# Performance work log

Measured on AMD Instinct MI355X. Metric: run time of the kernel, lower is better.

The kernel has to match this reference:

```python
import math
import jax, jax.numpy as jnp
import numpy as np

B, S, D, H = 4, 2048, 1024, 16
HD = D // H
NEG = float(jnp.finfo(jnp.float16).min)  # matches torch.finfo(torch.float16).min

def setup_inputs() -> dict:
    key = jax.random.key(0)
    ks = jax.random.split(key, 10)
    s = 1.0 / math.sqrt(D)
    return {
        "x": jax.random.normal(ks[0], (B, S, D), jnp.float32),
        "mask": jax.random.randint(ks[1], (B, 1, S, S), 0, 2).astype(bool),
        "Wq": jax.random.normal(ks[2], (D, D), jnp.float32) * s,
        "bq": jnp.zeros((D,), jnp.float32),
        "Wk": jax.random.normal(ks[3], (D, D), jnp.float32) * s,
        "bk": jnp.zeros((D,), jnp.float32),
        "Wv": jax.random.normal(ks[4], (D, D), jnp.float32) * s,
        "bv": jnp.zeros((D,), jnp.float32),
        "Wf": jax.random.normal(ks[5], (D, D), jnp.float32) * s,
        "bf": jnp.zeros((D,), jnp.float32),
    }

def reference(x, mask, Wq, bq, Wk, bk, Wv, bv, Wf, bf):
    b, s, d = x.shape
    # QKV projections (torch Linear: y = x @ W.T + b)
    q = (x @ Wq.T + bq).reshape(b, s, H, HD).transpose(0, 2, 1, 3)  # [b,h,s,hd]
    k = (x @ Wk.T + bk).reshape(b, s, H, HD).transpose(0, 2, 1, 3)
    v = (x @ Wv.T + bv).reshape(b, s, H, HD).transpose(0, 2, 1, 3)
    scores = jnp.einsum('bhqd,bhkd->bhqk', q, k) / math.sqrt(HD)
    scores = jnp.where(mask, scores, NEG)  # masked_fill_(~mask, fp16 min)
    p = jax.nn.softmax(scores, axis=-1)    # dropout is identity (eval / drop_rate=0)
    h = jnp.einsum('bhqk,bhkd->bhqd', p, v).transpose(0, 2, 1, 3).reshape(b, s, d)
    return h @ Wf.T + bf
```

## Files before the change

kernel.cpp:

```cpp
#include <hip/hip_runtime.h>
#include <math.h>

constexpr int S = 2048, D = 1024, H = 16;
constexpr float QSCL = 0.18033688011112042f;

typedef __attribute__((ext_vector_type(8))) short bf16x8;
typedef __attribute__((ext_vector_type(4))) short s16x4;
typedef __attribute__((ext_vector_type(4))) float f32x4;
typedef __attribute__((ext_vector_type(16))) float f32x16;

#define MFMA16(a,b,c) __builtin_amdgcn_mfma_f32_16x16x32_bf16(a,b,c,0,0,0)
#define MFMA32(a,b,c) __builtin_amdgcn_mfma_f32_32x32x16_bf16(a,b,c,0,0,0)

#if __has_builtin(__builtin_amdgcn_exp2f)
#define EXP2(x) __builtin_amdgcn_exp2f(x)
#else
#define EXP2(x) exp2f(x)
#endif

#define GLDS16(g, l) __builtin_amdgcn_global_load_lds( \
    (const __attribute__((address_space(1))) unsigned*)(const void*)(g), \
    (__attribute__((address_space(3))) unsigned*)(void*)(l), 16, 0, 0)

__device__ inline short f2bf(float f) {
    union { float f; unsigned u; } c; c.f = f;
    unsigned u = c.u + 0x7fffu + ((c.u >> 16) & 1u);
    return (short)(u >> 16);
}

__global__ __launch_bounds__(256)
void conv_pack(const float* __restrict__ x,  const float* __restrict__ wq,
               const float* __restrict__ wk, const float* __restrict__ wv,
               const float* __restrict__ wf,
               short* __restrict__ xb,  short* __restrict__ wqb,
               short* __restrict__ wkb, short* __restrict__ wvb,
               short* __restrict__ wfb)
{
    int i = blockIdx.x * 256 + threadIdx.x;
    const float* s; short* d; int o;
    if (i < 2097152) { s = x; d = xb; o = i; }
    else {
        int j = i - 2097152; int wsel = j >> 18; o = j & 262143;
        s = wsel == 0 ? wq : wsel == 1 ? wk : wsel == 2 ? wv : wf;
        d = wsel == 0 ? wqb : wsel == 1 ? wkb : wsel == 2 ? wvb : wfb;
    }
    float4 v = ((const float4*)s)[o];
    s16x4 r; r.x = f2bf(v.x); r.y = f2bf(v.y); r.z = f2bf(v.z); r.w = f2bf(v.w);
    ((s16x4*)d)[o] = r;
}

__global__ __launch_bounds__(256)
void conv_maskcol(const int* __restrict__ m, unsigned* __restrict__ o)
{
    int gid = blockIdx.x * 256 + threadIdx.x;
    int lane = gid & 63;
    int tile = (gid >> 6) & 31;
    int grp  = (gid >> 11) & 63;
    int bb   = gid >> 17;
    int qrow = grp * 32 + (lane & 31);
    int h = lane >> 5;
    const int* base = m + (size_t)bb * S * S + (size_t)qrow * S + tile * 64 + 4 * h;
    unsigned wbits = 0;
#pragma unroll
    for (int a = 0; a < 8; ++a) {
        int4 v = *(const int4*)(base + 8 * (a & 3) + 32 * (a >> 2));
        wbits |= (v.x != 0 ? 1u : 0u) << (4 * a);
        wbits |= (v.y != 0 ? 1u : 0u) << (4 * a + 1);
        wbits |= (v.z != 0 ? 1u : 0u) << (4 * a + 2);
        wbits |= (v.w != 0 ? 1u : 0u) << (4 * a + 3);
    }
    o[gid] = wbits;
}

__global__ __launch_bounds__(256, 3)
void qkv_mfma(const short* __restrict__ xb, const short* __restrict__ wcat,
              const float* __restrict__ bq, const float* __restrict__ bk,
              const float* __restrict__ bv,
              short* __restrict__ qo, short* __restrict__ ko, short* __restrict__ vto)
{
    __shared__ short As[128 * 64];
    __shared__ short Bs[128 * 64];
    const int t = threadIdx.x, lane = t & 63;
    const int w = __builtin_amdgcn_readfirstlane(t >> 6);
    const int lr = lane & 15, lg = lane >> 4;
    const int wr = w >> 1, wc = w & 1;
    const int m0 = blockIdx.x * 128, n0 = blockIdx.y * 128;

    const int srow = t >> 3;
    const int scol = ((t & 7) ^ (srow & 7)) * 8;
    const short* asrc = xb   + (size_t)(m0 + srow) * 1024 + scol;
    const short* bsrc = wcat + (size_t)(n0 + srow) * 1024 + scol;
    char* aldst = (char*)As + w * 1024;
    char* bldst = (char*)Bs + w * 1024;

    f32x4 z = {0.f, 0.f, 0.f, 0.f};
    f32x4 acc[4][4];
#pragma unroll
    for (int i = 0; i < 4; ++i)
#pragma unroll
        for (int jj = 0; jj < 4; ++jj) acc[i][jj] = z;

    for (int kt = 0; kt < 1024; kt += 64) {
        __syncthreads();
        GLDS16(asrc + kt,             aldst);
        GLDS16(asrc + kt + 32 * 1024, aldst + 4096);
        GLDS16(asrc + kt + 64 * 1024, aldst + 8192);
        GLDS16(asrc + kt + 96 * 1024, aldst + 12288);
        GLDS16(bsrc + kt,             bldst);
        GLDS16(bsrc + kt + 32 * 1024, bldst + 4096);
        GLDS16(bsrc + kt + 64 * 1024, bldst + 8192);
        GLDS16(bsrc + kt + 96 * 1024, bldst + 12288);
        __syncthreads();
#pragma unroll
        for (int ks = 0; ks < 2; ++ks) {
            bf16x8 af[4], bfr[4];
#pragma unroll
            for (int fi = 0; fi < 4; ++fi) {
                const int ra = wr * 64 + fi * 16 + lr;
                af[fi] = *(const bf16x8*)((const char*)As + ra * 128 +
                          ((ks * 64 + lg * 16) ^ ((ra & 7) << 4)));
                const int rb = wc * 64 + fi * 16 + lr;
                bfr[fi] = *(const bf16x8*)((const char*)Bs + rb * 128 +
                          ((ks * 64 + lg * 16) ^ ((rb & 7) << 4)));
            }
#pragma unroll
            for (int fi = 0; fi < 4; ++fi)
#pragma unroll
                for (int fj = 0; fj < 4; ++fj)
                    acc[fi][fj] = MFMA16(af[fi], bfr[fj], acc[fi][fj]);
        }
    }

    const int bb = m0 >> 11;
    const int ssb = (m0 & (S - 1)) + wr * 64 + lg * 4;
    const int mat = n0 >> 10;
    const int nbase = (n0 & 1023) + wc * 64;

    if (mat == 0) {
#pragma unroll
        for (int fj = 0; fj < 4; ++fj) {
            const int nl = nbase + fj * 16 + lr, hh = nl >> 6, hd = nl & 63;
            const float bi = bq[nl];
#pragma unroll
            for (int fi = 0; fi < 4; ++fi)
#pragma unroll
                for (int r = 0; r < 4; ++r)
                    qo[(((size_t)bb * H + hh) * S + ssb + fi * 16 + r) * 64 + hd] =
                        f2bf((acc[fi][fj][r] + bi) * QSCL);
        }
    } else if (mat == 1) {
#pragma unroll
        for (int fj = 0; fj < 4; ++fj) {
            const int nl = nbase + fj * 16 + lr, hh = nl >> 6, hd = nl & 63;
            const float bi = bk[nl];
#pragma unroll
            for (int fi = 0; fi < 4; ++fi)
#pragma unroll
                for (int r = 0; r < 4; ++r)
                    ko[(((size_t)bb * H + hh) * S + ssb + fi * 16 + r) * 64 + hd] =
                        f2bf(acc[fi][fj][r] + bi);
        }
    } else {
#pragma unroll
        for (int fj = 0; fj < 4; ++fj) {
            const int nl = nbase + fj * 16 + lr, hh = nl >> 6, hd = nl & 63;
            const float bi = bv[nl];
#pragma unroll
            for (int fi = 0; fi < 4; ++fi) {
                s16x4 pk;
#pragma unroll
                for (int r = 0; r < 4; ++r) pk[r] = f2bf(acc[fi][fj][r] + bi);
                *(s16x4*)(vto + (((size_t)bb * H + hh) * 64 + hd) * S + ssb + fi * 16) = pk;
            }
        }
    }
}

__global__ __launch_bounds__(256, 3)
void attn_mfma8(const short* __restrict__ qg, const short* __restrict__ kg,
                const short* __restrict__ vtg,
                const unsigned* __restrict__ mcol,
                short* __restrict__ hc)
{
    __shared__ short Kl[2][64 * 64];
    __shared__ short Vl[2][64 * 64];

    const int t = threadIdx.x, lane = t & 63;
    const int w = __builtin_amdgcn_readfirstlane(t >> 6);
    const int l31 = lane & 31, h = lane >> 5;

    const int id = blockIdx.x;
    const int xcd = id & 7, j = id >> 3;
    const int bh = xcd + 8 * (j >> 4);
    const int q0 = (j & 15) * 128;
    const int bb = bh >> 4, hh = bh & 15;

    const short* qb  = qg  + (size_t)bh * S * 64;
    const short* kb  = kg  + (size_t)bh * S * 64;
    const short* vtb = vtg + (size_t)bh * 64 * S;
    const unsigned* mc = mcol + ((size_t)(bb * 64 + (q0 >> 5) + w)) * 32 * 64 + lane;

    const int qrow = q0 + w * 32 + l31;
    bf16x8 qf[4];
#pragma unroll
    for (int ds = 0; ds < 4; ++ds)
        qf[ds] = *(const bf16x8*)(qb + (size_t)qrow * 64 + ds * 16 + 8 * h);

    const int sk = t >> 3;
    const int soff = (((t & 7) * 16) ^ ((sk & 7) << 4)) >> 1;
    const int rbyte = l31 * 128;
    const int sz = (lane & 7) << 4;

    f32x16 z16;
#pragma unroll
    for (int i = 0; i < 16; ++i) z16[i] = 0.f;
    f32x16 O0 = z16, O1 = z16;
    float li = 0.f;

    auto issue_stage = [&](int kt, int buf) {
        const short* ks0 = kb + (size_t)(kt + sk) * 64 + soff;
        const short* vs0 = vtb + (size_t)sk * S + kt + soff;
        char* kB = (char*)&Kl[buf][0] + w * 1024;
        char* vB = (char*)&Vl[buf][0] + w * 1024;
        GLDS16(ks0, kB);
        GLDS16(ks0 + 32 * 64, kB + 4096);
        GLDS16(vs0, vB);
        GLDS16(vs0 + (size_t)32 * S, vB + 4096);
    };

    unsigned mcw = mc[0];
    issue_stage(0, 0);
    __syncthreads();

    for (int tile = 0; tile < 32; ++tile) {
        const int cur = tile & 1;
        unsigned mcn = 0;
        if (tile < 31) {
            issue_stage((tile + 1) * 64, cur ^ 1);
            mcn = mc[(tile + 1) * 64];
        }

        f32x16 s0 = z16, s1 = z16;
        const char* Kb = (const char*)&Kl[cur][0];
#pragma unroll
        for (int ds = 0; ds < 4; ++ds) {
            const int off = ((ds * 32 + h * 16) ^ sz);
            bf16x8 a0 = *(const bf16x8*)(Kb + rbyte + off);
            bf16x8 a1 = *(const bf16x8*)(Kb + 4096 + rbyte + off);
            s0 = MFMA32(a0, qf[ds], s0);
            s1 = MFMA32(a1, qf[ds], s1);
        }

        const char* Vb = (const char*)&Vl[cur][0];
#pragma unroll
        for (int ks = 0; ks < 4; ++ks) {
            const int rb = (ks < 2) ? ks * 8 : (ks - 2) * 8;
            const int wb = (ks < 2) ? rb : 16 + rb;
            float pv[8];
#pragma unroll
            for (int jj = 0; jj < 8; ++jj) {
                float sv = (ks < 2) ? s0[rb + jj] : s1[rb + jj];
                sv = (mcw & (1u << (wb + jj))) ? sv : -INFINITY;
                pv[jj] = EXP2(sv);
                li += pv[jj];
            }
            int w0a, w1a, w0b, w1b;
            asm volatile("v_cvt_pk_bf16_f32 %0, %1, %2" : "=v"(w0a) : "v"(pv[0]), "v"(pv[1]));
            asm volatile("v_cvt_pk_bf16_f32 %0, %1, %2" : "=v"(w1a) : "v"(pv[2]), "v"(pv[3]));
            asm volatile("v_cvt_pk_bf16_f32 %0, %1, %2" : "=v"(w0b) : "v"(pv[4]), "v"(pv[5]));
            asm volatile("v_cvt_pk_bf16_f32 %0, %1, %2" : "=v"(w1b) : "v"(pv[6]), "v"(pv[7]));
            asm volatile("v_permlane32_swap_b32 %0, %1" : "+v"(w0a), "+v"(w0b));
            asm volatile("v_permlane32_swap_b32 %0, %1" : "+v"(w1a), "+v"(w1b));
            union { int i[4]; bf16x8 v; } pf;
            pf.i[0] = w0a; pf.i[1] = w1a; pf.i[2] = w0b; pf.i[3] = w1b;

            const int koff = ((ks * 32 + h * 16) ^ sz);
            bf16x8 v0 = *(const bf16x8*)(Vb + rbyte + koff);
            bf16x8 v1 = *(const bf16x8*)(Vb + 4096 + rbyte + koff);
            O0 = MFMA32(pf.v, v0, O0);
            O1 = MFMA32(pf.v, v1, O1);
        }

        if (tile < 31) mcw = mcn;
        __syncthreads();
    }

    li += __shfl_xor(li, 32);
    const float inv = 1.f / li;
    const int ib = __builtin_bit_cast(int, inv);
    const size_t outb = (size_t)bb * S * D + (size_t)hh * 64;
#pragma unroll
    for (int r = 0; r < 16; ++r) {
        const int qp = (r & 3) + 8 * (r >> 2);
        const int vlo = __builtin_amdgcn_readlane(ib, qp);
        const int vhi = __builtin_amdgcn_readlane(ib, qp + 4);
        const float ir = h ? __builtin_bit_cast(float, vhi)
                           : __builtin_bit_cast(float, vlo);
        const int row = q0 + w * 32 + qp + 4 * h;
        hc[outb + (size_t)row * D + l31]      = f2bf(O0[r] * ir);
        hc[outb + (size_t)row * D + 32 + l31] = f2bf(O1[r] * ir);
    }
}

__global__ __launch_bounds__(256, 3)
void proj_mfma(const short* __restrict__ hb, const short* __restrict__ wfb,
               const float* __restrict__ bfp, float* __restrict__ out)
{
    __shared__ short As[128 * 64];
    __shared__ short Bs[128 * 64];
    const int t = threadIdx.x, lane = t & 63;
    const int w = __builtin_amdgcn_readfirstlane(t >> 6);
    const int lr = lane & 15, lg = lane >> 4;
    const int wr = w >> 1, wc = w & 1;
    const int m0 = blockIdx.x * 128, n0 = blockIdx.y * 128;

    const int srow = t >> 3;
    const int scol = ((t & 7) ^ (srow & 7)) * 8;
    const short* asrc = hb  + (size_t)(m0 + srow) * 1024 + scol;
    const short* bsrc = wfb + (size_t)(n0 + srow) * 1024 + scol;
    char* aldst = (char*)As + w * 1024;
    char* bldst = (char*)Bs + w * 1024;

    f32x4 z = {0.f, 0.f, 0.f, 0.f};
    f32x4 acc[4][4];
#pragma unroll
    for (int i = 0; i < 4; ++i)
#pragma unroll
        for (int jj = 0; jj < 4; ++jj) acc[i][jj] = z;

    for (int kt = 0; kt < 1024; kt += 64) {
        __syncthreads();
        GLDS16(asrc + kt,             aldst);
        GLDS16(asrc + kt + 32 * 1024, aldst + 4096);
        GLDS16(asrc + kt + 64 * 1024, aldst + 8192);
        GLDS16(asrc + kt + 96 * 1024, aldst + 12288);
        GLDS16(bsrc + kt,             bldst);
        GLDS16(bsrc + kt + 32 * 1024, bldst + 4096);
        GLDS16(bsrc + kt + 64 * 1024, bldst + 8192);
        GLDS16(bsrc + kt + 96 * 1024, bldst + 12288);
        __syncthreads();
#pragma unroll
        for (int ks = 0; ks < 2; ++ks) {
            bf16x8 af[4], bfr[4];
#pragma unroll
            for (int fi = 0; fi < 4; ++fi) {
                const int ra = wr * 64 + fi * 16 + lr;
                af[fi] = *(const bf16x8*)((const char*)As + ra * 128 +
                          ((ks * 64 + lg * 16) ^ ((ra & 7) << 4)));
                const int rb = wc * 64 + fi * 16 + lr;
                bfr[fi] = *(const bf16x8*)((const char*)Bs + rb * 128 +
                          ((ks * 64 + lg * 16) ^ ((rb & 7) << 4)));
            }
#pragma unroll
            for (int fi = 0; fi < 4; ++fi)
#pragma unroll
                for (int fj = 0; fj < 4; ++fj)
                    acc[fi][fj] = MFMA16(af[fi], bfr[fj], acc[fi][fj]);
        }
    }

#pragma unroll
    for (int fj = 0; fj < 4; ++fj) {
        const int nl = n0 + wc * 64 + fj * 16 + lr;
        const float bi = bfp[nl];
#pragma unroll
        for (int fi = 0; fi < 4; ++fi)
#pragma unroll
            for (int r = 0; r < 4; ++r)
                out[(size_t)(m0 + wr * 64 + fi * 16 + lg * 4 + r) * 1024 + nl] =
                    acc[fi][fj][r] + bi;
    }
}

extern "C" void kernel_launch(void* const* d_in, const int* in_sizes, int n_in,
                              void* d_out, int out_size, void* d_ws, size_t ws_size,
                              hipStream_t stream)
{
    const float* x  = (const float*)d_in[0];
    const int* mask = (const int*)d_in[1];
    const float* Wq = (const float*)d_in[2];
    const float* bq = (const float*)d_in[3];
    const float* Wk = (const float*)d_in[4];
    const float* bk = (const float*)d_in[5];
    const float* Wv = (const float*)d_in[6];
    const float* bv = (const float*)d_in[7];
    const float* Wf = (const float*)d_in[8];
    const float* bf = (const float*)d_in[9];
    float* out = (float*)d_out;

    char* p = (char*)d_ws;
    short* xb  = (short*)p; p += 16777216;
    short* wqb = (short*)p; p += 2097152;
    short* wkb = (short*)p; p += 2097152;
    short* wvb = (short*)p; p += 2097152;
    short* wfb = (short*)p; p += 2097152;
    short* qb  = (short*)p; p += 16777216;
    short* kb  = (short*)p; p += 16777216;
    short* vtb = (short*)p; p += 16777216;
    short* hcb = (short*)p; p += 16777216;
    unsigned* mcol = (unsigned*)p; p += 2097152;

    conv_pack<<<12288, 256, 0, stream>>>(x, Wq, Wk, Wv, Wf, xb, wqb, wkb, wvb, wfb);
    conv_maskcol<<<2048, 256, 0, stream>>>(mask, mcol);
    qkv_mfma<<<dim3(64, 24), 256, 0, stream>>>(xb, wqb, bq, bk, bv, qb, kb, vtb);
    attn_mfma8<<<1024, 256, 0, stream>>>(qb, kb, vtb, mcol, hcb);
    proj_mfma<<<dim3(64, 8), 256, 0, stream>>>(hcb, wfb, bf, out);
}
```

Before: 195.0 us.

## Triple-buffer QKV GEMM with 256x128 tiles and 512-thread blocks

Replaces the single-buffered QKV projection GEMM with a three-stage LDS pipeline: global-to-LDS loads for k-step k+2 are issued while the MFMAs for step k run, using vmcnt waits and a single barrier per iteration. Each block grows to 256 rows by 128 columns with 8 waves sharing the B tile, and the k-step shrinks to 32. MFMA issue is wrapped in s_setprio. The intent is to hide global memory latency and halve the B-tile traffic per output. In exchange it uses 72KB of LDS per block, which limits occupancy, and relies on hand-placed waitcnt counts being correct.

```diff
diff --git a/kernel.cpp b/kernel.cpp
--- a/kernel.cpp
+++ b/kernel.cpp
@@ -72,26 +72,28 @@
     o[gid] = wbits;
 }
 
-__global__ __launch_bounds__(256, 3)
-void qkv_mfma(const short* __restrict__ xb, const short* __restrict__ wcat,
-              const float* __restrict__ bq, const float* __restrict__ bk,
-              const float* __restrict__ bv,
-              short* __restrict__ qo, short* __restrict__ ko, short* __restrict__ vto)
-{
-    __shared__ short As[128 * 64];
-    __shared__ short Bs[128 * 64];
+__global__ __launch_bounds__(512, 2)
+void qkv_p3(const short* __restrict__ xb, const short* __restrict__ wcat,
+            const float* __restrict__ bq, const float* __restrict__ bk,
+            const float* __restrict__ bv,
+            short* __restrict__ qo, short* __restrict__ ko, short* __restrict__ vto)
+{
+    __shared__ char Lds[73728];
+
     const int t = threadIdx.x, lane = t & 63;
-    const int w = __builtin_amdgcn_readfirstlane(t >> 6);
+    const int wu = __builtin_amdgcn_readfirstlane(t >> 6);
     const int lr = lane & 15, lg = lane >> 4;
-    const int wr = w >> 1, wc = w & 1;
-    const int m0 = blockIdx.x * 128, n0 = blockIdx.y * 128;
-
-    const int srow = t >> 3;
-    const int scol = ((t & 7) ^ (srow & 7)) * 8;
-    const short* asrc = xb   + (size_t)(m0 + srow) * 1024 + scol;
-    const short* bsrc = wcat + (size_t)(n0 + srow) * 1024 + scol;
-    char* aldst = (char*)As + w * 1024;
-    char* bldst = (char*)Bs + w * 1024;
+    const int wr = wu >> 1, wc = wu & 1;
+    const int m0 = blockIdx.x * 256, n0 = blockIdx.y * 128;
+
+    const int srow = t >> 2;
+    const int sw   = ((t & 3) ^ (srow & 3)) * 8;
+    const short* asrc0 = xb   + (size_t)(m0 + srow) * 1024 + sw;
+    const short* bsrc0 = wcat + (size_t)(n0 + srow) * 1024 + sw;
+
+    const int colA  = (lg * 16) ^ ((lr & 3) << 4);
+    const int aRowB = (wr * 64 + lr) * 64;
+    const int bRowB = (wc * 64 + lr) * 64;
 
     f32x4 z = {0.f, 0.f, 0.f, 0.f};
     f32x4 acc[4][4];
@@ -100,39 +102,51 @@
 #pragma unroll
         for (int jj = 0; jj < 4; ++jj) acc[i][jj] = z;
 
-    for (int kt = 0; kt < 1024; kt += 64) {
-        __syncthreads();
-        GLDS16(asrc + kt,             aldst);
-        GLDS16(asrc + kt + 32 * 1024, aldst + 4096);
-        GLDS16(asrc + kt + 64 * 1024, aldst + 8192);
-        GLDS16(asrc + kt + 96 * 1024, aldst + 12288);
-        GLDS16(bsrc + kt,             bldst);
-        GLDS16(bsrc + kt + 32 * 1024, bldst + 4096);
-        GLDS16(bsrc + kt + 64 * 1024, bldst + 8192);
-        GLDS16(bsrc + kt + 96 * 1024, bldst + 12288);
-        __syncthreads();
-#pragma unroll
-        for (int ks = 0; ks < 2; ++ks) {
-            bf16x8 af[4], bfr[4];
-#pragma unroll
-            for (int fi = 0; fi < 4; ++fi) {
-                const int ra = wr * 64 + fi * 16 + lr;
-                af[fi] = *(const bf16x8*)((const char*)As + ra * 128 +
-                          ((ks * 64 + lg * 16) ^ ((ra & 7) << 4)));
-                const int rb = wc * 64 + fi * 16 + lr;
-                bfr[fi] = *(const bf16x8*)((const char*)Bs + rb * 128 +
-                          ((ks * 64 + lg * 16) ^ ((rb & 7) << 4)));
-            }
-#pragma unroll
-            for (int fi = 0; fi < 4; ++fi)
-#pragma unroll
-                for (int fj = 0; fj < 4; ++fj)
-                    acc[fi][fj] = MFMA16(af[fi], bfr[fj], acc[fi][fj]);
-        }
+    auto stage = [&](int k2, int buf2) {
+        const int kofs = k2 * 32;
+        char* ab = Lds + buf2 * 16384 + wu * 1024;
+        char* bb = Lds + 49152 + buf2 * 8192 + wu * 1024;
+        GLDS16(asrc0 + kofs, ab);
+        GLDS16(asrc0 + kofs + 128 * 1024, ab + 8192);
+        GLDS16(bsrc0 + kofs, bb);
+    };
+
+    stage(0, 0);
+    stage(1, 1);
+    asm volatile("s_waitcnt vmcnt(3)" ::: "memory");
+    __builtin_amdgcn_s_barrier();
+    __builtin_amdgcn_sched_barrier(0);
+
+    for (int k = 0; k < 32; ++k) {
+        const int buf = k % 3;
+        if (k + 2 < 32) stage(k + 2, (k + 2) % 3);
+
+        const char* Ab = Lds + buf * 16384;
+        const char* Bb = Lds + 49152 + buf * 8192;
+        bf16x8 bfr[4], af[4];
+#pragma unroll
+        for (int fj = 0; fj < 4; ++fj)
+            bfr[fj] = *(const bf16x8*)(Bb + bRowB + fj * 1024 + colA);
+#pragma unroll
+        for (int fi = 0; fi < 4; ++fi)
+            af[fi] = *(const bf16x8*)(Ab + aRowB + fi * 1024 + colA);
+
+        __builtin_amdgcn_s_setprio(1);
+#pragma unroll
+        for (int fi = 0; fi < 4; ++fi)
+#pragma unroll
+            for (int fj = 0; fj < 4; ++fj)
+                acc[fi][fj] = MFMA16(af[fi], bfr[fj], acc[fi][fj]);
+        __builtin_amdgcn_s_setprio(0);
+
+        if (k < 30)       asm volatile("s_waitcnt vmcnt(3)" ::: "memory");
+        else if (k == 30) asm volatile("s_waitcnt vmcnt(0)" ::: "memory");
+        __builtin_amdgcn_s_barrier();
+        __builtin_amdgcn_sched_barrier(0);
     }
 
     const int bb = m0 >> 11;
-    const int ssb = (m0 & (S - 1)) + wr * 64 + lg * 4;
+    const int ssb = (m0 & 2047) + wr * 64 + lg * 4;
     const int mat = n0 >> 10;
     const int nbase = (n0 & 1023) + wc * 64;
 
@@ -402,7 +416,7 @@
 
     conv_pack<<<12288, 256, 0, stream>>>(x, Wq, Wk, Wv, Wf, xb, wqb, wkb, wvb, wfb);
     conv_maskcol<<<2048, 256, 0, stream>>>(mask, mcol);
-    qkv_mfma<<<dim3(64, 24), 256, 0, stream>>>(xb, wqb, bq, bk, bv, qb, kb, vtb);
+    qkv_p3<<<dim3(32, 24), 512, 0, stream>>>(xb, wqb, bq, bk, bv, qb, kb, vtb);
     attn_mfma8<<<1024, 256, 0, stream>>>(qb, kb, vtb, mcol, hcb);
     proj_mfma<<<dim3(64, 8), 256, 0, stream>>>(hcb, wfb, bf, out);
 }
```

After: 194.9 us. Within noise of the previous version (-0.0%).
